# Performance work log

Measured on AMD Instinct MI355X. Metric: run time of the kernel, lower is better.

The kernel has to match this reference:

```python
import jax, jax.numpy as jnp
import numpy as np

INSIZE = 1024
OUTSIZE = 1024
N_U = 20
N_V = 20
SIGMA_MIN = 0.6
SIGMA_MAX = 1.0
R = (SIGMA_MAX - SIGMA_MIN) / 2.0
SIGMA_MEAN = SIGMA_MIN + R
BATCH = 32768


def setup_inputs() -> dict:
    key = jax.random.key(0)
    k_x, k_U, k_p, k_V = jax.random.split(key, 4)
    x = jax.random.normal(k_x, (BATCH, INSIZE), dtype=jnp.float32)
    U = jnp.triu(jax.random.normal(k_U, (INSIZE, INSIZE), dtype=jnp.float32))
    V = jnp.triu(jax.random.normal(k_V, (OUTSIZE, OUTSIZE), dtype=jnp.float32))
    nsigma = min(INSIZE, OUTSIZE)
    p = 0.001 * jax.random.normal(k_p, (nsigma,), dtype=jnp.float32)
    bias = jnp.zeros((OUTSIZE,), dtype=jnp.float32)
    return {"x": x, "U": U, "p": p, "V": V, "bias": bias}


def _hprod(x, u, k):
    # x: [bs, dim], u: [dim], k static int. Householder reflection on the trailing k coords.
    xs = x[:, -k:]                     # [bs, k]
    us = u[-k:]                        # [k]
    alpha = 2.0 * (xs @ us) / jnp.sum(us * us)   # [bs]
    xs_new = xs - alpha[:, None] * us[None, :]
    if k < x.shape[1]:
        return jnp.concatenate([x[:, :-k], xs_new], axis=1)
    return xs_new


def _sigma_matrix(p):
    sigmas = 2.0 * R * (jax.nn.sigmoid(p) - 0.5) + SIGMA_MEAN   # [nsigma]
    nsigma = p.shape[0]
    S = jnp.zeros((INSIZE, OUTSIZE), dtype=p.dtype)
    idx = jnp.arange(nsigma)
    return S.at[idx, idx].set(sigmas)


def reference(x, U, p, V, bias):
    # U multiply: reflectors 0..N_U-1 with k = insize - i
    for i in range(N_U):
        x = _hprod(x, U[i], INSIZE - i)
    x = x @ _sigma_matrix(p)
    # V multiply: reflectors N_V-1..0 with k = outsize - i
    for i in range(N_V - 1, -1, -1):
        x = _hprod(x, V[i], OUTSIZE - i)
    return x + bias
```

## Files before the change

kernel.cpp:

```cpp
#include <hip/hip_runtime.h>
#include <hip/hip_bf16.h>

typedef __attribute__((ext_vector_type(8))) short bf16x8;
typedef __attribute__((ext_vector_type(4))) short bf16x4;
typedef __attribute__((ext_vector_type(4))) float f32x4;

#define NU 20

__device__ __forceinline__ float b2f(unsigned short u) {
    union { float f; unsigned v; } x; x.v = ((unsigned)u) << 16; return x.f;
}
__device__ __forceinline__ unsigned short f2b(float f) {
    union { float f; unsigned v; } x; x.f = f;
    unsigned r = x.v + 0x7FFF + ((x.v >> 16) & 1);
    return (unsigned short)(r >> 16);
}


__global__ __launch_bounds__(256) void k_gram(
        const float* __restrict__ U, const float* __restrict__ p,
        const float* __restrict__ V, const float* __restrict__ bias,
        float* __restrict__ GU, float* __restrict__ GV,
        float* __restrict__ s_ws, float* __restrict__ b_ws) {
    const int b = blockIdx.x, T = threadIdx.x;
    if (b >= 420) {
        int t = (b - 420) * 256 + T;
        float pv = p[t];
        s_ws[t] = 0.4f / (1.0f + __expf(-pv)) + 0.6f;
        b_ws[t] = bias[t];
        return;
    }
    const float* M = (b < 210) ? U : V;
    float* Gm = (b < 210) ? GU : GV;
    int i = (b < 210) ? b : b - 210;
    int k = 0;
    while ((k + 1) * (k + 2) / 2 <= i) k++;
    int j = i - k * (k + 1) / 2;
    f32x4 a4 = *(const f32x4*)&M[j * 1024 + T * 4];
    f32x4 b4 = *(const f32x4*)&M[k * 1024 + T * 4];
    float acc = a4[0] * b4[0] + a4[1] * b4[1] + a4[2] * b4[2] + a4[3] * b4[3];
    for (int off = 32; off; off >>= 1) acc += __shfl_down(acc, off, 64);
    __shared__ float part[4];
    if ((T & 63) == 0) part[T >> 6] = acc;
    __syncthreads();
    if (T == 0) {
        float s = part[0] + part[1] + part[2] + part[3];
        Gm[j * 20 + k] = s; Gm[k * 20 + j] = s;
    }
}

__global__ __launch_bounds__(256) void k_recur(
        const float* __restrict__ U, const float* __restrict__ V,
        const float* __restrict__ GUg, const float* __restrict__ GVg,
        const float* __restrict__ s_ws,
        float* __restrict__ A, float* __restrict__ Csc,
        unsigned short* __restrict__ Ft, unsigned short* __restrict__ G) {
    __shared__ float sGU[400], sGV[400];
    const int T = threadIdx.x;
    const int t = blockIdx.x * 256 + T;
    for (int i = T; i < 400; i += 256) { sGU[i] = GUg[i]; sGV[i] = GVg[i]; }
    __syncthreads();
    float sig = s_ws[t];
    float a[NU], c[NU];
    for (int k = 0; k < NU; k++) {
        float w = U[k * 1024 + t];
        for (int j = 0; j < k; j++) w -= a[j] * sGU[j * 20 + k];
        a[k] = (2.0f / sGU[k * 20 + k]) * w;
    }
    for (int k = NU - 1; k >= 0; k--) {
        float w = V[k * 1024 + t];
        for (int j = k + 1; j < NU; j++) w -= c[j] * sGV[j * 20 + k];
        c[k] = (2.0f / sGV[k * 20 + k]) * w;
    }
    for (int k = 0; k < NU; k++) { A[k * 1024 + t] = a[k]; Ft[k * 1024 + t] = f2b(a[k]); }
    for (int b = 0; b < NU; b++) Csc[b * 1024 + t] = sig * c[b];
    for (int k = 2 * NU; k < 64; k++) Ft[k * 1024 + t] = 0;
    for (int k = 0; k < NU; k++) G[t * 64 + k] = f2b(sig * U[k * 1024 + t]);
    for (int k = 0; k < NU; k++) G[t * 64 + NU + k] = f2b(V[k * 1024 + t]);
    for (int k = 2 * NU; k < 64; k++) G[t * 64 + k] = 0;
}

__global__ __launch_bounds__(256) void k_e(
        const float* __restrict__ U, const float* __restrict__ Csc,
        float* __restrict__ E) {
    const int aa = blockIdx.x / 20, bb = blockIdx.x % 20;
    const int T = threadIdx.x;
    f32x4 a4 = *(const f32x4*)&U[aa * 1024 + T * 4];
    f32x4 b4 = *(const f32x4*)&Csc[bb * 1024 + T * 4];
    float acc = a4[0] * b4[0] + a4[1] * b4[1] + a4[2] * b4[2] + a4[3] * b4[3];
    for (int off = 32; off; off >>= 1) acc += __shfl_down(acc, off, 64);
    __shared__ float part[4];
    if ((T & 63) == 0) part[T >> 6] = acc;
    __syncthreads();
    if (T == 0) E[aa * 20 + bb] = part[0] + part[1] + part[2] + part[3];
}

__global__ __launch_bounds__(256) void k_f2(
        const float* __restrict__ A, const float* __restrict__ Csc,
        const float* __restrict__ Eg, unsigned short* __restrict__ Ft) {
    __shared__ float sE[400];
    const int T = threadIdx.x;
    const int t = blockIdx.x * 256 + T;
    for (int i = T; i < 400; i += 256) sE[i] = Eg[i];
    __syncthreads();
    float av[NU];
    for (int a = 0; a < NU; a++) av[a] = A[a * 1024 + t];
    for (int b = 0; b < NU; b++) {
        float v = Csc[b * 1024 + t];
        for (int a = 0; a < NU; a++) v -= av[a] * sE[a * 20 + b];
        Ft[(NU + b) * 1024 + t] = f2b(v);
    }
}

__global__ __launch_bounds__(256, 2) void k_main(
        const float* __restrict__ x, const unsigned short* __restrict__ Ft,
        const unsigned short* __restrict__ G, const float* __restrict__ s_ws,
        const float* __restrict__ b_ws, float* __restrict__ out) {
    __shared__ __align__(16) char sm[36864];
    unsigned short* xb0 = (unsigned short*)sm;
    unsigned short* xb1 = (unsigned short*)(sm + 9216);
    unsigned short* fb0 = (unsigned short*)(sm + 18432);
    unsigned short* fb1 = (unsigned short*)(sm + 27648);
    unsigned short* rl = fb0;
    unsigned short* gl = (unsigned short*)sm;

    const int T = threadIdx.x;
    const int m0 = blockIdx.x * 64;
    const int wv = T >> 6, lane = T & 63;
    const int mc = lane & 15, quad = lane >> 4;

    f32x4 acc1[4];
    for (int i = 0; i < 4; i++) acc1[i] = (f32x4){0.f, 0.f, 0.f, 0.f};

#define STAGE_A(k0, xd, fd)                                                     \
    {                                                                           \
        for (int i = 0; i < 4; i++) {                                           \
            int e = i * 1024 + T * 4;                                           \
            int row = e >> 6, col = e & 63;                                     \
            f32x4 xv = *(const f32x4*)&x[(size_t)(m0 + row) * 1024 + (k0) + col];\
            bf16x4 xc;                                                          \
            for (int j = 0; j < 4; j++) xc[j] = (short)f2b(xv[j]);              \
            *(bf16x4*)&(xd)[row * 72 + col] = xc;                               \
        }                                                                       \
        for (int i = 0; i < 2; i++) {                                           \
            int e = i * 2048 + T * 8;                                           \
            int row = e >> 6, col = e & 63;                                     \
            *(bf16x8*)&(fd)[row * 72 + col] =                                   \
                *(const bf16x8*)&Ft[row * 1024 + (k0) + col];                   \
        }                                                                       \
    }

    STAGE_A(0, xb0, fb0);
    for (int kt = 0; kt < 16; kt++) {
        __syncthreads();
        if (kt < 15) {
            if ((kt + 1) & 1) STAGE_A((kt + 1) * 64, xb1, fb1)
            else              STAGE_A((kt + 1) * 64, xb0, fb0)
        }
        const unsigned short* xl = (kt & 1) ? xb1 : xb0;
        const unsigned short* fl = (kt & 1) ? fb1 : fb0;
        for (int kk = 0; kk < 64; kk += 32) {
            bf16x8 af = *(const bf16x8*)&xl[(wv * 16 + mc) * 72 + kk + quad * 8];
            for (int nt = 0; nt < 4; nt++) {
                bf16x8 bfr = *(const bf16x8*)&fl[(nt * 16 + mc) * 72 + kk + quad * 8];
                acc1[nt] = __builtin_amdgcn_mfma_f32_16x16x32_bf16(af, bfr, acc1[nt], 0, 0, 0);
            }
        }
    }
    {
        const int rrow = wv * 16 + quad * 4;
        for (int nt = 0; nt < 4; nt++)
            for (int rg = 0; rg < 4; rg++)
                rl[(rrow + rg) * 72 + nt * 16 + mc] = f2b(acc1[nt][rg]);
    }

    for (int nt0 = 0; nt0 < 1024; nt0 += 128) {
        __syncthreads();
        for (int i = 0; i < 4; i++) {
            int e = i * 2048 + T * 8;
            int n = e >> 6, k = e & 63;
            *(bf16x8*)&gl[n * 72 + k] = *(const bf16x8*)&G[(size_t)(nt0 + n) * 64 + k];
        }
        __syncthreads();
        f32x4 acc2[8];
        for (int i = 0; i < 8; i++) acc2[i] = (f32x4){0.f, 0.f, 0.f, 0.f};
        for (int kk = 0; kk < 64; kk += 32) {
            bf16x8 af = *(const bf16x8*)&rl[(wv * 16 + mc) * 72 + kk + quad * 8];
            for (int nf = 0; nf < 8; nf++) {
                bf16x8 bfr = *(const bf16x8*)&gl[(nf * 16 + mc) * 72 + kk + quad * 8];
                acc2[nf] = __builtin_amdgcn_mfma_f32_16x16x32_bf16(af, bfr, acc2[nf], 0, 0, 0);
            }
        }
        for (int nf = 0; nf < 8; nf++) {
            int col = nt0 + nf * 16 + mc;
            float sv = s_ws[col], bv = b_ws[col];
            size_t base = (size_t)(m0 + wv * 16 + quad * 4) * 1024 + col;
            out[base]        = x[base]        * sv - acc2[nf][0] + bv;
            out[base + 1024] = x[base + 1024] * sv - acc2[nf][1] + bv;
            out[base + 2048] = x[base + 2048] * sv - acc2[nf][2] + bv;
            out[base + 3072] = x[base + 3072] * sv - acc2[nf][3] + bv;
        }
    }
#undef STAGE_A
}

extern "C" void kernel_launch(void* const* d_in, const int* in_sizes, int n_in,
                              void* d_out, int out_size, void* d_ws, size_t ws_size,
                              hipStream_t stream) {
    const float* x    = (const float*)d_in[0];
    const float* U    = (const float*)d_in[1];
    const float* p    = (const float*)d_in[2];
    const float* V    = (const float*)d_in[3];
    const float* bias = (const float*)d_in[4];

    char* ws = (char*)d_ws;
    unsigned short* Ft = (unsigned short*)ws;
    unsigned short* G  = (unsigned short*)(ws + 131072);
    float* s_ws        = (float*)(ws + 262144);
    float* b_ws        = (float*)(ws + 266240);
    float* GU          = (float*)(ws + 270336);
    float* GV          = (float*)(ws + 274432);
    float* A           = (float*)(ws + 278528);
    float* Csc         = (float*)(ws + 360448);
    float* E           = (float*)(ws + 442368);
    float* out = (float*)d_out;

    hipLaunchKernelGGL(k_gram,  dim3(424), dim3(256), 0, stream, U, p, V, bias, GU, GV, s_ws, b_ws);
    hipLaunchKernelGGL(k_recur, dim3(4),   dim3(256), 0, stream, U, V, GU, GV, s_ws, A, Csc, Ft, G);
    hipLaunchKernelGGL(k_e,     dim3(400), dim3(256), 0, stream, U, Csc, E);
    hipLaunchKernelGGL(k_f2,    dim3(4),   dim3(256), 0, stream, A, Csc, E, Ft);
    hipLaunchKernelGGL(k_main,  dim3(512), dim3(256), 0, stream, x, Ft, G, s_ws, b_ws, out);
}
```

Before: 294.5 us.

## Restructure main kernel to 16-row blocks with split-K across waves

The main low-rank kernel now gives each block 16 rows instead of 64 and splits the K=1024 reduction across the four waves. Each wave streams x and Ft straight from global into registers with a two-step prefetch, so the LDS staging tiles and the per-tile barriers are gone. Partial results are summed through shared memory, and each wave then handles a quarter of the output columns, reading G directly from global. This quadruples the grid, raises the occupancy target, and cuts LDS traffic and synchronisation. In exchange, G and Ft are re-read from global or cache by four times as many blocks.

```diff
diff --git a/kernel.cpp b/kernel.cpp
--- a/kernel.cpp
+++ b/kernel.cpp
@@ -112,96 +112,108 @@
     }
 }
 
-__global__ __launch_bounds__(256, 2) void k_main(
+__global__ __launch_bounds__(256, 4) void k_main(
         const float* __restrict__ x, const unsigned short* __restrict__ Ft,
         const unsigned short* __restrict__ G, const float* __restrict__ s_ws,
         const float* __restrict__ b_ws, float* __restrict__ out) {
-    __shared__ __align__(16) char sm[36864];
-    unsigned short* xb0 = (unsigned short*)sm;
-    unsigned short* xb1 = (unsigned short*)(sm + 9216);
-    unsigned short* fb0 = (unsigned short*)(sm + 18432);
-    unsigned short* fb1 = (unsigned short*)(sm + 27648);
-    unsigned short* rl = fb0;
-    unsigned short* gl = (unsigned short*)sm;
-
-    const int T = threadIdx.x;
-    const int m0 = blockIdx.x * 64;
+    __shared__ __align__(16) float sA[4][16][64];
+    __shared__ __align__(16) unsigned short rl[16][72];
+
+    const int T = threadIdx.x;
     const int wv = T >> 6, lane = T & 63;
     const int mc = lane & 15, quad = lane >> 4;
+    const int m0 = blockIdx.x * 16;
 
     f32x4 acc1[4];
+#pragma unroll
     for (int i = 0; i < 4; i++) acc1[i] = (f32x4){0.f, 0.f, 0.f, 0.f};
 
-#define STAGE_A(k0, xd, fd)                                                     \
-    {                                                                           \
-        for (int i = 0; i < 4; i++) {                                           \
-            int e = i * 1024 + T * 4;                                           \
-            int row = e >> 6, col = e & 63;                                     \
-            f32x4 xv = *(const f32x4*)&x[(size_t)(m0 + row) * 1024 + (k0) + col];\
-            bf16x4 xc;                                                          \
-            for (int j = 0; j < 4; j++) xc[j] = (short)f2b(xv[j]);              \
-            *(bf16x4*)&(xd)[row * 72 + col] = xc;                               \
-        }                                                                       \
-        for (int i = 0; i < 2; i++) {                                           \
-            int e = i * 2048 + T * 8;                                           \
-            int row = e >> 6, col = e & 63;                                     \
-            *(bf16x8*)&(fd)[row * 72 + col] =                                   \
-                *(const bf16x8*)&Ft[row * 1024 + (k0) + col];                   \
-        }                                                                       \
-    }
-
-    STAGE_A(0, xb0, fb0);
-    for (int kt = 0; kt < 16; kt++) {
-        __syncthreads();
-        if (kt < 15) {
-            if ((kt + 1) & 1) STAGE_A((kt + 1) * 64, xb1, fb1)
-            else              STAGE_A((kt + 1) * 64, xb0, fb0)
-        }
-        const unsigned short* xl = (kt & 1) ? xb1 : xb0;
-        const unsigned short* fl = (kt & 1) ? fb1 : fb0;
-        for (int kk = 0; kk < 64; kk += 32) {
-            bf16x8 af = *(const bf16x8*)&xl[(wv * 16 + mc) * 72 + kk + quad * 8];
-            for (int nt = 0; nt < 4; nt++) {
-                bf16x8 bfr = *(const bf16x8*)&fl[(nt * 16 + mc) * 72 + kk + quad * 8];
-                acc1[nt] = __builtin_amdgcn_mfma_f32_16x16x32_bf16(af, bfr, acc1[nt], 0, 0, 0);
-            }
-        }
-    }
+    const float* xp = &x[(size_t)(m0 + mc) * 1024 + wv * 256 + quad * 8];
+    const unsigned short* fp = &Ft[(size_t)mc * 1024 + wv * 256 + quad * 8];
+
+    f32x4 xa0 = *(const f32x4*)(xp);
+    f32x4 xb0 = *(const f32x4*)(xp + 4);
+    f32x4 xa1 = *(const f32x4*)(xp + 32);
+    f32x4 xb1 = *(const f32x4*)(xp + 36);
+    bf16x8 f0 = *(const bf16x8*)(fp);
+    bf16x8 f1 = *(const bf16x8*)(fp + 16384);
+    bf16x8 f2 = *(const bf16x8*)(fp + 32768);
+    bf16x8 f3 = *(const bf16x8*)(fp + 49152);
+
+#pragma unroll
+    for (int ks = 0; ks < 8; ks++) {
+        f32x4 xa2, xb2; bf16x8 n0, n1, n2, n3;
+        if (ks < 6) {
+            const float* xq = xp + (ks + 2) * 32;
+            xa2 = *(const f32x4*)(xq);
+            xb2 = *(const f32x4*)(xq + 4);
+        }
+        if (ks < 7) {
+            const unsigned short* fq = fp + (ks + 1) * 32;
+            n0 = *(const bf16x8*)(fq);
+            n1 = *(const bf16x8*)(fq + 16384);
+            n2 = *(const bf16x8*)(fq + 32768);
+            n3 = *(const bf16x8*)(fq + 49152);
+        }
+        bf16x8 af;
+#pragma unroll
+        for (int j = 0; j < 4; j++) {
+            af[j]     = (short)f2b(xa0[j]);
+            af[j + 4] = (short)f2b(xb0[j]);
+        }
+        acc1[0] = __builtin_amdgcn_mfma_f32_16x16x32_bf16(af, f0, acc1[0], 0, 0, 0);
+        acc1[1] = __builtin_amdgcn_mfma_f32_16x16x32_bf16(af, f1, acc1[1], 0, 0, 0);
+        acc1[2] = __builtin_amdgcn_mfma_f32_16x16x32_bf16(af, f2, acc1[2], 0, 0, 0);
+        acc1[3] = __builtin_amdgcn_mfma_f32_16x16x32_bf16(af, f3, acc1[3], 0, 0, 0);
+        if (ks < 7) {
+            xa0 = xa1; xb0 = xb1;
+            f0 = n0; f1 = n1; f2 = n2; f3 = n3;
+        }
+        if (ks < 6) { xa1 = xa2; xb1 = xb2; }
+    }
+
+#pragma unroll
+    for (int nt = 0; nt < 4; nt++)
+#pragma unroll
+        for (int rg = 0; rg < 4; rg++)
+            sA[wv][quad * 4 + rg][nt * 16 + mc] = acc1[nt][rg];
+    __syncthreads();
+
     {
-        const int rrow = wv * 16 + quad * 4;
-        for (int nt = 0; nt < 4; nt++)
-            for (int rg = 0; rg < 4; rg++)
-                rl[(rrow + rg) * 72 + nt * 16 + mc] = f2b(acc1[nt][rg]);
-    }
-
-    for (int nt0 = 0; nt0 < 1024; nt0 += 128) {
-        __syncthreads();
-        for (int i = 0; i < 4; i++) {
-            int e = i * 2048 + T * 8;
-            int n = e >> 6, k = e & 63;
-            *(bf16x8*)&gl[n * 72 + k] = *(const bf16x8*)&G[(size_t)(nt0 + n) * 64 + k];
-        }
-        __syncthreads();
-        f32x4 acc2[8];
-        for (int i = 0; i < 8; i++) acc2[i] = (f32x4){0.f, 0.f, 0.f, 0.f};
-        for (int kk = 0; kk < 64; kk += 32) {
-            bf16x8 af = *(const bf16x8*)&rl[(wv * 16 + mc) * 72 + kk + quad * 8];
-            for (int nf = 0; nf < 8; nf++) {
-                bf16x8 bfr = *(const bf16x8*)&gl[(nf * 16 + mc) * 72 + kk + quad * 8];
-                acc2[nf] = __builtin_amdgcn_mfma_f32_16x16x32_bf16(af, bfr, acc2[nf], 0, 0, 0);
-            }
-        }
-        for (int nf = 0; nf < 8; nf++) {
-            int col = nt0 + nf * 16 + mc;
-            float sv = s_ws[col], bv = b_ws[col];
-            size_t base = (size_t)(m0 + wv * 16 + quad * 4) * 1024 + col;
-            out[base]        = x[base]        * sv - acc2[nf][0] + bv;
-            out[base + 1024] = x[base + 1024] * sv - acc2[nf][1] + bv;
-            out[base + 2048] = x[base + 2048] * sv - acc2[nf][2] + bv;
-            out[base + 3072] = x[base + 3072] * sv - acc2[nf][3] + bv;
-        }
-    }
-#undef STAGE_A
+        const int row = T >> 4, c0 = (T & 15) * 4;
+        f32x4 v = *(const f32x4*)&sA[0][row][c0];
+#pragma unroll
+        for (int w = 1; w < 4; w++) {
+            f32x4 u = *(const f32x4*)&sA[w][row][c0];
+            v[0] += u[0]; v[1] += u[1]; v[2] += u[2]; v[3] += u[3];
+        }
+        bf16x4 rv;
+#pragma unroll
+        for (int j = 0; j < 4; j++) rv[j] = (short)f2b(v[j]);
+        *(bf16x4*)&rl[row][c0] = rv;
+    }
+    __syncthreads();
+
+    bf16x8 pa0 = *(const bf16x8*)&rl[mc][quad * 8];
+    bf16x8 pa1 = *(const bf16x8*)&rl[mc][32 + quad * 8];
+    const int C0 = wv * 256;
+
+#pragma unroll 2
+    for (int nf = 0; nf < 16; nf++) {
+        const int col = C0 + nf * 16 + mc;
+        const unsigned short* gp = &G[(size_t)col * 64 + quad * 8];
+        bf16x8 g0 = *(const bf16x8*)(gp);
+        bf16x8 g1 = *(const bf16x8*)(gp + 32);
+        f32x4 a = (f32x4){0.f, 0.f, 0.f, 0.f};
+        a = __builtin_amdgcn_mfma_f32_16x16x32_bf16(pa0, g0, a, 0, 0, 0);
+        a = __builtin_amdgcn_mfma_f32_16x16x32_bf16(pa1, g1, a, 0, 0, 0);
+        const float sv = s_ws[col], bv = b_ws[col];
+        size_t base = (size_t)(m0 + quad * 4) * 1024 + col;
+        out[base]        = x[base]        * sv - a[0] + bv;
+        out[base + 1024] = x[base + 1024] * sv - a[1] + bv;
+        out[base + 2048] = x[base + 2048] * sv - a[2] + bv;
+        out[base + 3072] = x[base + 3072] * sv - a[3] + bv;
+    }
 }
 
 extern "C" void kernel_launch(void* const* d_in, const int* in_sizes, int n_in,
@@ -225,9 +237,9 @@
     float* E           = (float*)(ws + 442368);
     float* out = (float*)d_out;
 
-    hipLaunchKernelGGL(k_gram,  dim3(424), dim3(256), 0, stream, U, p, V, bias, GU, GV, s_ws, b_ws);
-    hipLaunchKernelGGL(k_recur, dim3(4),   dim3(256), 0, stream, U, V, GU, GV, s_ws, A, Csc, Ft, G);
-    hipLaunchKernelGGL(k_e,     dim3(400), dim3(256), 0, stream, U, Csc, E);
-    hipLaunchKernelGGL(k_f2,    dim3(4),   dim3(256), 0, stream, A, Csc, E, Ft);
-    hipLaunchKernelGGL(k_main,  dim3(512), dim3(256), 0, stream, x, Ft, G, s_ws, b_ws, out);
-}
+    hipLaunchKernelGGL(k_gram,  dim3(424),  dim3(256), 0, stream, U, p, V, bias, GU, GV, s_ws, b_ws);
+    hipLaunchKernelGGL(k_recur, dim3(4),    dim3(256), 0, stream, U, V, GU, GV, s_ws, A, Csc, Ft, G);
+    hipLaunchKernelGGL(k_e,     dim3(400),  dim3(256), 0, stream, U, Csc, E);
+    hipLaunchKernelGGL(k_f2,    dim3(4),    dim3(256), 0, stream, A, Csc, E, Ft);
+    hipLaunchKernelGGL(k_main,  dim3(2048), dim3(256), 0, stream, x, Ft, G, s_ws, b_ws, out);
+}
```

Result: slower. 314.4 us (+6.8%).
